# Performance work log

Hardware: AMD Instinct MI355X
Metric: run time of the kernel (lower is better)

Reference implementation:

```python
import jax, jax.numpy as jnp
import numpy as np

NUM_HEADS = 16

def setup_inputs() -> dict:
    key = jax.random.key(0)
    ks = jax.random.split(key, 5)
    E = 1024
    x = jax.random.normal(ks[0], (2, 2048, E), dtype=jnp.float32)
    w_in = jax.random.normal(ks[1], (3 * E, E), dtype=jnp.float32) * (E ** -0.5)
    b_in = jax.random.normal(ks[2], (3 * E,), dtype=jnp.float32) * 0.02
    w_out = jax.random.normal(ks[3], (E, E), dtype=jnp.float32) * (E ** -0.5)
    b_out = jax.random.normal(ks[4], (E,), dtype=jnp.float32) * 0.02
    return {"x": x, "w_in": w_in, "b_in": b_in, "w_out": w_out, "b_out": b_out}


def reference(x, w_in, b_in, w_out, b_out):
    B, N, E = x.shape
    H = NUM_HEADS
    Dh = E // H
    # fused QKV projection (torch Linear: x @ W^T + b)
    qkv = x @ w_in.T + b_in                      # [B, N, 3E]
    q, k, v = jnp.split(qkv, 3, axis=-1)
    # [B, H, N, Dh]
    q = q.reshape(B, N, H, Dh).transpose(0, 2, 1, 3)
    k = k.reshape(B, N, H, Dh).transpose(0, 2, 1, 3)
    v = v.reshape(B, N, H, Dh).transpose(0, 2, 1, 3)
    scale = Dh ** -0.5
    scores = jnp.einsum("bhqd,bhkd->bhqk", q, k) * scale  # [B, H, N, N]
    attn = jax.nn.softmax(scores, axis=-1)
    out = jnp.einsum("bhqk,bhkd->bhqd", attn, v)          # [B, H, N, Dh]
    out = out.transpose(0, 2, 1, 3).reshape(B, N, E)
    return out @ w_out.T + b_out
```

## Files before the change

### kernel.cpp

```cpp
#include <hip/hip_runtime.h>


typedef __bf16 bf16;
typedef __bf16 bf16x8 __attribute__((ext_vector_type(8)));
typedef __bf16 bf16x4 __attribute__((ext_vector_type(4)));
typedef float  f32x4  __attribute__((ext_vector_type(4)));

#define MFMA16(a, b, c) __builtin_amdgcn_mfma_f32_16x16x32_bf16((a), (b), (c), 0, 0, 0)

#define SC2 0.18033688011112042f

__device__ __forceinline__ void gld_lds16(const void* g, void* l) {
  __builtin_amdgcn_global_load_lds((const __attribute__((address_space(1))) void*)g,
                                   (__attribute__((address_space(3))) void*)l,
                                   16, 0, 0);
}

__device__ __forceinline__ float exp2_raw(float x) {
  float r;
  asm("v_exp_f32 %0, %1" : "=v"(r) : "v"(x));
  return r;
}

__global__ __launch_bounds__(256) void cast3_kernel(
    const float* __restrict__ x, const float* __restrict__ wi,
    const float* __restrict__ wo, bf16* __restrict__ xb,
    bf16* __restrict__ wib, bf16* __restrict__ wob) {
  const int i = (blockIdx.x * 256 + threadIdx.x) * 4;
  const float* s; bf16* d; int off;
  if (i < 4194304)      { s = x;  d = xb;  off = i; }
  else if (i < 7340032) { s = wi; d = wib; off = i - 4194304; }
  else                  { s = wo; d = wob; off = i - 7340032; }
  const float4 v = *(const float4*)(s + off);
  bf16x4 o;
  o[0] = (bf16)v.x; o[1] = (bf16)v.y; o[2] = (bf16)v.z; o[3] = (bf16)v.w;
  *(bf16x4*)(d + off) = o;
}

__global__ __launch_bounds__(256) void gemm_qkv_kernel(
    const bf16* __restrict__ A,
    const bf16* __restrict__ B,
    const float* __restrict__ bias,
    bf16* __restrict__ qb, bf16* __restrict__ kb, bf16* __restrict__ vb) {
  constexpr int K = 1024;
  __shared__ __align__(16) char smem[128 * 136 * 2];
  const int tid  = threadIdx.x;
  const int lane = tid & 63;
  const int wave = tid >> 6;
  const int m0 = blockIdx.y * 128;
  const int n0 = blockIdx.x * 128;
  const int r_ = tid >> 2;
  const int k_ = (tid & 3) * 8;
  const int lr = lane & 15, lg = lane >> 4;
  const int wm = (wave >> 1) * 64, wn = (wave & 1) * 64;

  f32x4 acc[4][4];
#pragma unroll
  for (int i = 0; i < 4; ++i)
#pragma unroll
    for (int j = 0; j < 4; ++j) acc[i][j] = (f32x4){0.f, 0.f, 0.f, 0.f};

  {
    gld_lds16(A + (size_t)(m0 + r_) * K + k_,      smem + tid * 16);
    gld_lds16(A + (size_t)(m0 + 64 + r_) * K + k_, smem + 4096 + tid * 16);
    gld_lds16(B + (size_t)(n0 + r_) * K + k_,      smem + 16384 + tid * 16);
    gld_lds16(B + (size_t)(n0 + 64 + r_) * K + k_, smem + 20480 + tid * 16);
  }

  int buf = 0;
  for (int t = 0; t < 32; ++t) {
    __syncthreads();
    char* Ac = smem + buf * 8192;
    char* Bc = smem + 16384 + buf * 8192;
    if (t + 1 < 32) {
      const int k0 = (t + 1) * 32;
      char* An = smem + (buf ^ 1) * 8192;
      char* Bn = smem + 16384 + (buf ^ 1) * 8192;
      gld_lds16(A + (size_t)(m0 + r_) * K + k0 + k_,      An + tid * 16);
      gld_lds16(A + (size_t)(m0 + 64 + r_) * K + k0 + k_, An + 4096 + tid * 16);
      gld_lds16(B + (size_t)(n0 + r_) * K + k0 + k_,      Bn + tid * 16);
      gld_lds16(B + (size_t)(n0 + 64 + r_) * K + k0 + k_, Bn + 4096 + tid * 16);
    }

    bf16x8 af[4], bfr[4];
#pragma unroll
    for (int i = 0; i < 4; ++i)
      af[i] = *(const bf16x8*)(Ac + (size_t)((wm + i * 16 + lr) * 32 + lg * 8) * 2);
#pragma unroll
    for (int j = 0; j < 4; ++j)
      bfr[j] = *(const bf16x8*)(Bc + (size_t)((wn + j * 16 + lr) * 32 + lg * 8) * 2);
    __builtin_amdgcn_s_setprio(1);
#pragma unroll
    for (int i = 0; i < 4; ++i)
#pragma unroll
      for (int j = 0; j < 4; ++j) acc[i][j] = MFMA16(af[i], bfr[j], acc[i][j]);
    __builtin_amdgcn_s_setprio(0);
    buf ^= 1;
  }

  __syncthreads();
  bf16* T = (bf16*)smem;
  const int which = n0 >> 10;
  const int wi0 = n0 & 1023;
  const int bb = m0 >> 11, nn0 = m0 & 2047;

  if (which < 2) {
    const float scl = (which == 0) ? SC2 : 1.0f;
#pragma unroll
    for (int j = 0; j < 4; ++j) {
      const int tcol = wn + j * 16 + lr;
      const float bv = bias[n0 + tcol];
#pragma unroll
      for (int i = 0; i < 4; ++i)
#pragma unroll
        for (int r = 0; r < 4; ++r) {
          const int trow = wm + i * 16 + lg * 4 + r;
          T[trow * 136 + tcol] = (bf16)((acc[i][j][r] + bv) * scl);
        }
    }
    __syncthreads();
    bf16* dst = (which == 0) ? qb : kb;
    const int l = tid & 15, g = tid >> 4;
    const int cc = l * 8;
    const int h = (wi0 + cc) >> 6, d = cc & 63;
#pragma unroll
    for (int p = 0; p < 8; ++p) {
      const int rr = p * 16 + g;
      *(bf16x8*)(dst + ((size_t)(bb * 16 + h) * 2048 + nn0 + rr) * 64 + d) =
          *(const bf16x8*)(T + rr * 136 + cc);
    }
  } else {
#pragma unroll
    for (int j = 0; j < 4; ++j) {
      const int c = wn + j * 16 + lr;
      const float bv = bias[n0 + c];
#pragma unroll
      for (int i = 0; i < 4; ++i)
#pragma unroll
        for (int r = 0; r < 4; ++r) {
          const int rr = wm + i * 16 + lg * 4 + r;
          T[c * 136 + rr] = (bf16)(acc[i][j][r] + bv);
        }
    }
    __syncthreads();
    const int l = tid & 15, g = tid >> 4;
    const int nof = l * 8;
#pragma unroll
    for (int p = 0; p < 8; ++p) {
      const int c = p * 16 + g;
      const int h = (wi0 + c) >> 6, d = (wi0 + c) & 63;
      *(bf16x8*)(vb + ((size_t)(bb * 16 + h) * 64 + d) * 2048 + nn0 + nof) =
          *(const bf16x8*)(T + c * 136 + nof);
    }
  }
}

__global__ __launch_bounds__(512) void flash_attn_kernel(
    const bf16* __restrict__ q, const bf16* __restrict__ k,
    const bf16* __restrict__ vt, bf16* __restrict__ o) {
  __shared__ bf16 Ks[2][64 * 64];
  __shared__ bf16 Vs[2][64 * 64];
  __shared__ bf16 Pl[8][16 * 64];

  const int tid  = threadIdx.x;
  const int lane = tid & 63;
  const int wave = tid >> 6;
  const int lr = lane & 15, lg = lane >> 4;
  const int id   = blockIdx.x;
  const int slot = id >> 3;
  const int bh   = (id & 7) * 4 + (slot >> 4);
  const int qt   = slot & 15;
  const bf16* qp = q  + (size_t)bh * (2048 * 64);
  const bf16* kp = k  + (size_t)bh * (2048 * 64);
  const bf16* vp = vt + (size_t)bh * (64 * 2048);
  const int q0 = qt * 128 + wave * 16;
  const int wmask = (lr & 7) << 4;

  const int L = tid * 16;
  const int srow = L >> 7;
  const int scol = ((L & 127) ^ ((srow & 7) << 4)) >> 1;

  bf16x8 qf[2];
#pragma unroll
  for (int t = 0; t < 2; ++t)
    qf[t] = *(const bf16x8*)(qp + (size_t)(q0 + lr) * 64 + t * 32 + lg * 8);

  bf16x8 ones;
#pragma unroll
  for (int i = 0; i < 8; ++i) ones[i] = (bf16)1.0f;

  f32x4 oacc[4];
#pragma unroll
  for (int j = 0; j < 4; ++j) oacc[j] = (f32x4){0.f, 0.f, 0.f, 0.f};
  f32x4 lacc = (f32x4){0.f, 0.f, 0.f, 0.f};

  gld_lds16(kp + (size_t)srow * 64 + scol,       (char*)Ks[0] + L);
  gld_lds16(vp + (size_t)srow * 2048 + 0 + scol, (char*)Vs[0] + L);
  __syncthreads();

  int buf = 0;
  for (int t = 0; t < 32; ++t) {
    if (t + 1 < 32) {
      const int nkv = t * 64 + 64;
      gld_lds16(kp + (size_t)(nkv + srow) * 64 + scol, (char*)Ks[buf ^ 1] + L);
      gld_lds16(vp + (size_t)srow * 2048 + nkv + scol, (char*)Vs[buf ^ 1] + L);
    }

    f32x4 s[4];
#pragma unroll
    for (int sub = 0; sub < 4; ++sub) s[sub] = (f32x4){0.f, 0.f, 0.f, 0.f};
    __builtin_amdgcn_s_setprio(1);
#pragma unroll
    for (int sub = 0; sub < 4; ++sub) {
#pragma unroll
      for (int tt = 0; tt < 2; ++tt) {
        const int row = sub * 16 + lr;
        const int byte = (row << 7) + (((tt * 32 + lg * 8) << 1) ^ ((row & 7) << 4));
        bf16x8 kf = *(const bf16x8*)((const char*)Ks[buf] + byte);
        s[sub] = MFMA16(kf, qf[tt], s[sub]);
      }
    }
    __builtin_amdgcn_s_setprio(0);

    {
      char* pl = (char*)&Pl[wave][0] + lr * 128;
#pragma unroll
      for (int sub = 0; sub < 4; ++sub) {
        const float e0 = exp2_raw(s[sub][0]);
        const float e1 = exp2_raw(s[sub][1]);
        const float e2 = exp2_raw(s[sub][2]);
        const float e3 = exp2_raw(s[sub][3]);
        unsigned p01, p23;
        asm("v_cvt_pk_bf16_f32 %0, %1, %2" : "=v"(p01) : "v"(e0), "v"(e1));
        asm("v_cvt_pk_bf16_f32 %0, %1, %2" : "=v"(p23) : "v"(e2), "v"(e3));
        uint2 w; w.x = p01; w.y = p23;
        *(uint2*)(pl + ((sub * 32 + lg * 8) ^ wmask)) = w;
      }
    }
    bf16x8 pa[2];
#pragma unroll
    for (int kk = 0; kk < 2; ++kk)
      pa[kk] = *(const bf16x8*)((const char*)&Pl[wave][0] + lr * 128 +
                                ((kk * 64 + lg * 16) ^ wmask));

    __builtin_amdgcn_s_setprio(1);
#pragma unroll
    for (int j = 0; j < 4; ++j) {
#pragma unroll
      for (int kk = 0; kk < 2; ++kk) {
        const int row = j * 16 + lr;
        const int byte = (row << 7) + (((kk * 32 + lg * 8) << 1) ^ ((row & 7) << 4));
        bf16x8 vf = *(const bf16x8*)((const char*)Vs[buf] + byte);
        oacc[j] = MFMA16(pa[kk], vf, oacc[j]);
      }
    }
#pragma unroll
    for (int kk = 0; kk < 2; ++kk) lacc = MFMA16(pa[kk], ones, lacc);
    __builtin_amdgcn_s_setprio(0);

    __syncthreads();
    buf ^= 1;
  }

  const int b = bh >> 4, h = bh & 15;
  float inv[4];
#pragma unroll
  for (int r = 0; r < 4; ++r) inv[r] = 1.f / lacc[r];
#pragma unroll
  for (int j = 0; j < 4; ++j) {
#pragma unroll
    for (int r = 0; r < 4; ++r) {
      const int qrow = q0 + lg * 4 + r;
      o[((size_t)(b * 2048 + qrow)) * 1024 + h * 64 + j * 16 + lr] =
          (bf16)(oacc[j][r] * inv[r]);
    }
  }
}

__global__ __launch_bounds__(256) void gemm_out_kernel(
    const bf16* __restrict__ A,
    const bf16* __restrict__ B,
    const float* __restrict__ bias,
    float* __restrict__ out) {
  constexpr int K = 1024;
  __shared__ __align__(16) char smem[32768];
  const int tid  = threadIdx.x;
  const int lane = tid & 63;
  const int wave = tid >> 6;
  const int m0 = blockIdx.y * 128;
  const int n0 = blockIdx.x * 128;
  const int r_ = tid >> 2;
  const int k_ = (tid & 3) * 8;
  const int lr = lane & 15, lg = lane >> 4;
  const int wm = (wave >> 1) * 64, wn = (wave & 1) * 64;

  f32x4 acc[4][4];
#pragma unroll
  for (int i = 0; i < 4; ++i)
#pragma unroll
    for (int j = 0; j < 4; ++j) acc[i][j] = (f32x4){0.f, 0.f, 0.f, 0.f};

  {
    gld_lds16(A + (size_t)(m0 + r_) * K + k_,      smem + tid * 16);
    gld_lds16(A + (size_t)(m0 + 64 + r_) * K + k_, smem + 4096 + tid * 16);
    gld_lds16(B + (size_t)(n0 + r_) * K + k_,      smem + 16384 + tid * 16);
    gld_lds16(B + (size_t)(n0 + 64 + r_) * K + k_, smem + 20480 + tid * 16);
  }

  int buf = 0;
  for (int t = 0; t < 32; ++t) {
    __syncthreads();
    char* Ac = smem + buf * 8192;
    char* Bc = smem + 16384 + buf * 8192;
    if (t + 1 < 32) {
      const int k0 = (t + 1) * 32;
      char* An = smem + (buf ^ 1) * 8192;
      char* Bn = smem + 16384 + (buf ^ 1) * 8192;
      gld_lds16(A + (size_t)(m0 + r_) * K + k0 + k_,      An + tid * 16);
      gld_lds16(A + (size_t)(m0 + 64 + r_) * K + k0 + k_, An + 4096 + tid * 16);
      gld_lds16(B + (size_t)(n0 + r_) * K + k0 + k_,      Bn + tid * 16);
      gld_lds16(B + (size_t)(n0 + 64 + r_) * K + k0 + k_, Bn + 4096 + tid * 16);
    }

    bf16x8 af[4], bfr[4];
#pragma unroll
    for (int i = 0; i < 4; ++i)
      af[i] = *(const bf16x8*)(Ac + (size_t)((wm + i * 16 + lr) * 32 + lg * 8) * 2);
#pragma unroll
    for (int j = 0; j < 4; ++j)
      bfr[j] = *(const bf16x8*)(Bc + (size_t)((wn + j * 16 + lr) * 32 + lg * 8) * 2);
    __builtin_amdgcn_s_setprio(1);
#pragma unroll
    for (int i = 0; i < 4; ++i)
#pragma unroll
      for (int j = 0; j < 4; ++j) acc[i][j] = MFMA16(af[i], bfr[j], acc[i][j]);
    __builtin_amdgcn_s_setprio(0);
    buf ^= 1;
  }

#pragma unroll
  for (int j = 0; j < 4; ++j) {
    const int col = n0 + wn + j * 16 + lr;
    const float bv = bias[col];
#pragma unroll
    for (int i = 0; i < 4; ++i) {
#pragma unroll
      for (int r = 0; r < 4; ++r) {
        const int row = m0 + wm + i * 16 + lg * 4 + r;
        out[(size_t)row * 1024 + col] = acc[i][j][r] + bv;
      }
    }
  }
}

extern "C" void kernel_launch(void* const* d_in, const int* in_sizes, int n_in,
                              void* d_out, int out_size, void* d_ws, size_t ws_size,
                              hipStream_t stream) {
  const float* x     = (const float*)d_in[0];
  const float* w_in  = (const float*)d_in[1];
  const float* b_in  = (const float*)d_in[2];
  const float* w_out = (const float*)d_in[3];
  const float* b_out = (const float*)d_in[4];
  float* out = (float*)d_out;

  char* ws = (char*)d_ws;
  const size_t MB = 1ull << 20;
  bf16* xb  = (bf16*)(ws + 0 * MB);
  bf16* wib = (bf16*)(ws + 8 * MB);
  bf16* wob = (bf16*)(ws + 14 * MB);
  bf16* qb  = (bf16*)(ws + 16 * MB);
  bf16* kb  = (bf16*)(ws + 24 * MB);
  bf16* vb  = (bf16*)(ws + 32 * MB);
  bf16* ab  = (bf16*)(ws + 40 * MB);

  cast3_kernel<<<dim3(8192), dim3(256), 0, stream>>>(x, w_in, w_out, xb, wib, wob);
  gemm_qkv_kernel<<<dim3(24, 32), dim3(256), 0, stream>>>(xb, wib, b_in, qb, kb, vb);
  flash_attn_kernel<<<dim3(512), dim3(512), 0, stream>>>(qb, kb, vb, ab);
  gemm_out_kernel<<<dim3(8, 32), dim3(256), 0, stream>>>(ab, wob, b_out, out);
}
```

Measured before the change: 188.7 us.

## Triple-buffer K/V in flash attention and halve out-GEMM row tile

The attention kernel now keeps three K/V LDS buffers and prefetches two tiles ahead. It waits with an explicit vmcnt and one barrier per iteration instead of a trailing __syncthreads, which is meant to hide global-load latency better. The output projection GEMM uses 64-row tiles and twice as many blocks to fill more CUs. In exchange, LDS use rises in attention, and the GEMM loses some operand reuse per block.

```diff
diff --git a/kernel.cpp b/kernel.cpp
--- a/kernel.cpp
+++ b/kernel.cpp
@@ -158,8 +158,8 @@
 __global__ __launch_bounds__(512) void flash_attn_kernel(
     const bf16* __restrict__ q, const bf16* __restrict__ k,
     const bf16* __restrict__ vt, bf16* __restrict__ o) {
-  __shared__ bf16 Ks[2][64 * 64];
-  __shared__ bf16 Vs[2][64 * 64];
+  __shared__ bf16 Ks[3][64 * 64];
+  __shared__ bf16 Vs[3][64 * 64];
   __shared__ bf16 Pl[8][16 * 64];
 
   const int tid  = threadIdx.x;
@@ -194,18 +194,12 @@
   for (int j = 0; j < 4; ++j) oacc[j] = (f32x4){0.f, 0.f, 0.f, 0.f};
   f32x4 lacc = (f32x4){0.f, 0.f, 0.f, 0.f};
 
-  gld_lds16(kp + (size_t)srow * 64 + scol,       (char*)Ks[0] + L);
-  gld_lds16(vp + (size_t)srow * 2048 + 0 + scol, (char*)Vs[0] + L);
-  __syncthreads();
-
-  int buf = 0;
-  for (int t = 0; t < 32; ++t) {
-    if (t + 1 < 32) {
-      const int nkv = t * 64 + 64;
-      gld_lds16(kp + (size_t)(nkv + srow) * 64 + scol, (char*)Ks[buf ^ 1] + L);
-      gld_lds16(vp + (size_t)srow * 2048 + nkv + scol, (char*)Vs[buf ^ 1] + L);
-    }
-
+  auto stage = [&](int ti, int bi) {
+    gld_lds16(kp + (size_t)(ti * 64 + srow) * 64 + scol, (char*)Ks[bi] + L);
+    gld_lds16(vp + (size_t)srow * 2048 + ti * 64 + scol, (char*)Vs[bi] + L);
+  };
+
+  auto compute = [&](int cb) {
     f32x4 s[4];
 #pragma unroll
     for (int sub = 0; sub < 4; ++sub) s[sub] = (f32x4){0.f, 0.f, 0.f, 0.f};
@@ -216,7 +210,7 @@
       for (int tt = 0; tt < 2; ++tt) {
         const int row = sub * 16 + lr;
         const int byte = (row << 7) + (((tt * 32 + lg * 8) << 1) ^ ((row & 7) << 4));
-        bf16x8 kf = *(const bf16x8*)((const char*)Ks[buf] + byte);
+        bf16x8 kf = *(const bf16x8*)((const char*)Ks[cb] + byte);
         s[sub] = MFMA16(kf, qf[tt], s[sub]);
       }
     }
@@ -250,17 +244,29 @@
       for (int kk = 0; kk < 2; ++kk) {
         const int row = j * 16 + lr;
         const int byte = (row << 7) + (((kk * 32 + lg * 8) << 1) ^ ((row & 7) << 4));
-        bf16x8 vf = *(const bf16x8*)((const char*)Vs[buf] + byte);
+        bf16x8 vf = *(const bf16x8*)((const char*)Vs[cb] + byte);
         oacc[j] = MFMA16(pa[kk], vf, oacc[j]);
       }
     }
 #pragma unroll
     for (int kk = 0; kk < 2; ++kk) lacc = MFMA16(pa[kk], ones, lacc);
     __builtin_amdgcn_s_setprio(0);
-
-    __syncthreads();
-    buf ^= 1;
-  }
+  };
+
+  stage(0, 0);
+  stage(1, 1);
+
+  for (int t = 0; t < 31; ++t) {
+    asm volatile("s_waitcnt vmcnt(2)" ::: "memory");
+    __builtin_amdgcn_s_barrier();
+    __builtin_amdgcn_sched_barrier(0);
+    if (t + 2 < 32) stage(t + 2, (t + 2) % 3);
+    compute(t % 3);
+  }
+  asm volatile("s_waitcnt vmcnt(0)" ::: "memory");
+  __builtin_amdgcn_s_barrier();
+  __builtin_amdgcn_sched_barrier(0);
+  compute(31 % 3);
 
   const int b = bh >> 4, h = bh & 15;
   float inv[4];
@@ -283,55 +289,53 @@
     const float* __restrict__ bias,
     float* __restrict__ out) {
   constexpr int K = 1024;
-  __shared__ __align__(16) char smem[32768];
+  __shared__ __align__(16) char smem[24576];
   const int tid  = threadIdx.x;
   const int lane = tid & 63;
   const int wave = tid >> 6;
-  const int m0 = blockIdx.y * 128;
+  const int m0 = blockIdx.y * 64;
   const int n0 = blockIdx.x * 128;
   const int r_ = tid >> 2;
   const int k_ = (tid & 3) * 8;
   const int lr = lane & 15, lg = lane >> 4;
-  const int wm = (wave >> 1) * 64, wn = (wave & 1) * 64;
-
-  f32x4 acc[4][4];
-#pragma unroll
-  for (int i = 0; i < 4; ++i)
+  const int wm = (wave >> 1) * 32, wn = (wave & 1) * 64;
+
+  f32x4 acc[2][4];
+#pragma unroll
+  for (int i = 0; i < 2; ++i)
 #pragma unroll
     for (int j = 0; j < 4; ++j) acc[i][j] = (f32x4){0.f, 0.f, 0.f, 0.f};
 
   {
     gld_lds16(A + (size_t)(m0 + r_) * K + k_,      smem + tid * 16);
-    gld_lds16(A + (size_t)(m0 + 64 + r_) * K + k_, smem + 4096 + tid * 16);
-    gld_lds16(B + (size_t)(n0 + r_) * K + k_,      smem + 16384 + tid * 16);
-    gld_lds16(B + (size_t)(n0 + 64 + r_) * K + k_, smem + 20480 + tid * 16);
+    gld_lds16(B + (size_t)(n0 + r_) * K + k_,      smem + 8192 + tid * 16);
+    gld_lds16(B + (size_t)(n0 + 64 + r_) * K + k_, smem + 12288 + tid * 16);
   }
 
   int buf = 0;
   for (int t = 0; t < 32; ++t) {
     __syncthreads();
-    char* Ac = smem + buf * 8192;
-    char* Bc = smem + 16384 + buf * 8192;
+    char* Ac = smem + buf * 4096;
+    char* Bc = smem + 8192 + buf * 8192;
     if (t + 1 < 32) {
       const int k0 = (t + 1) * 32;
-      char* An = smem + (buf ^ 1) * 8192;
-      char* Bn = smem + 16384 + (buf ^ 1) * 8192;
+      char* An = smem + (buf ^ 1) * 4096;
+      char* Bn = smem + 8192 + (buf ^ 1) * 8192;
       gld_lds16(A + (size_t)(m0 + r_) * K + k0 + k_,      An + tid * 16);
-      gld_lds16(A + (size_t)(m0 + 64 + r_) * K + k0 + k_, An + 4096 + tid * 16);
       gld_lds16(B + (size_t)(n0 + r_) * K + k0 + k_,      Bn + tid * 16);
       gld_lds16(B + (size_t)(n0 + 64 + r_) * K + k0 + k_, Bn + 4096 + tid * 16);
     }
 
-    bf16x8 af[4], bfr[4];
-#pragma unroll
-    for (int i = 0; i < 4; ++i)
+    bf16x8 af[2], bfr[4];
+#pragma unroll
+    for (int i = 0; i < 2; ++i)
       af[i] = *(const bf16x8*)(Ac + (size_t)((wm + i * 16 + lr) * 32 + lg * 8) * 2);
 #pragma unroll
     for (int j = 0; j < 4; ++j)
       bfr[j] = *(const bf16x8*)(Bc + (size_t)((wn + j * 16 + lr) * 32 + lg * 8) * 2);
     __builtin_amdgcn_s_setprio(1);
 #pragma unroll
-    for (int i = 0; i < 4; ++i)
+    for (int i = 0; i < 2; ++i)
 #pragma unroll
       for (int j = 0; j < 4; ++j) acc[i][j] = MFMA16(af[i], bfr[j], acc[i][j]);
     __builtin_amdgcn_s_setprio(0);
@@ -343,7 +347,7 @@
     const int col = n0 + wn + j * 16 + lr;
     const float bv = bias[col];
 #pragma unroll
-    for (int i = 0; i < 4; ++i) {
+    for (int i = 0; i < 2; ++i) {
 #pragma unroll
       for (int r = 0; r < 4; ++r) {
         const int row = m0 + wm + i * 16 + lg * 4 + r;
@@ -376,5 +380,5 @@
   cast3_kernel<<<dim3(8192), dim3(256), 0, stream>>>(x, w_in, w_out, xb, wib, wob);
   gemm_qkv_kernel<<<dim3(24, 32), dim3(256), 0, stream>>>(xb, wib, b_in, qb, kb, vb);
   flash_attn_kernel<<<dim3(512), dim3(512), 0, stream>>>(qb, kb, vb, ab);
-  gemm_out_kernel<<<dim3(8, 32), dim3(256), 0, stream>>>(ab, wob, b_out, out);
-}
+  gemm_out_kernel<<<dim3(8, 64), dim3(256), 0, stream>>>(ab, wob, b_out, out);
+}
```

After: 185.0 us. Within noise of the previous version (-1.9%).
